# Optimization experiments

Hardware: AMD Instinct MI355X
Metric: run time of the kernel (lower is better)

The kernel has to match this reference:

```python
import jax, jax.numpy as jnp
import numpy as np

B, S, D_MODEL, D_FF, E, K = 4, 2048, 1024, 4096, 8, 2
CAP_FACTOR = 1.0


def setup_inputs() -> dict:
    key = jax.random.key(0)
    ks = jax.random.split(key, 6)
    std = 0.02
    return {
        "x": jax.random.normal(ks[0], (B, S, D_MODEL), jnp.float32),
        "router_w": jax.random.normal(ks[1], (E, D_MODEL), jnp.float32) * std,  # Linear(d_model,E,bias=False) weight
        "w1": jax.random.normal(ks[2], (E, D_MODEL, D_FF), jnp.float32) * std,
        "b1": jnp.zeros((E, D_FF), jnp.float32),
        "w2": jax.random.normal(ks[3], (E, D_FF, D_MODEL), jnp.float32) * std,
        "b2": jnp.zeros((E, D_MODEL), jnp.float32),
    }


def reference(x, router_w, w1, b1, w2, b2):
    b, s, d = x.shape
    T = b * s
    e = router_w.shape[0]
    capacity = int(CAP_FACTOR * T / e)  # static
    xf = x.reshape(T, d)

    # --- routing ---
    logits = xf @ router_w.T                       # [T,E]
    probs = jax.nn.softmax(logits, axis=-1)
    vals, idx = jax.lax.top_k(probs, K)            # [T,K] values / expert ids
    vals = vals / vals.sum(-1, keepdims=True)

    # dense gate matrix [T,E]; top_k experts are distinct so this is a scatter of K weights per token
    ar = jnp.arange(T)
    gates = jnp.zeros((T, e), x.dtype).at[ar[:, None], idx].add(vals)

    # --- load-balancing loss ---
    counts = jnp.zeros((e,), jnp.float32).at[idx.reshape(-1)].add(1.0)
    ideal = T * K / e
    lb_loss = jnp.sum((counts - ideal) ** 2) / (T ** 2)

    # --- capacity-limited dispatch (first `capacity` tokens in token order per expert) ---
    mask = gates > 0                                               # [T,E]
    order = jnp.argsort(jnp.logical_not(mask), axis=0)[:capacity]  # stable: assigned tokens first, ascending token id -> [cap,E]
    valid = jnp.take_along_axis(mask, order, axis=0)               # [cap,E] token actually assigned & within capacity
    idx_ec = order.T                                               # [E,cap]

    # --- grouped expert MLP ---
    xg = xf[idx_ec]                                                # [E,cap,D]
    h = jax.nn.gelu(jnp.einsum('ecd,edf->ecf', xg, w1) + b1[:, None, :], approximate=False)
    y = jnp.einsum('ecf,efd->ecd', h, w2) + b2[:, None, :]         # [E,cap,D]

    # --- combine (scatter-add with routing weights; dropped/invalid slots get weight 0) ---
    wt = gates[idx_ec, jnp.arange(e)[:, None]] * valid.T           # [E,cap]
    out = jnp.zeros((T, d), x.dtype).at[idx_ec.reshape(-1)].add((y * wt[..., None]).reshape(-1, d))
    return out.reshape(b, s, d), lb_loss
```

## Files before the change

kernel.cpp:

```cpp
#include <hip/hip_runtime.h>
#include <hip/hip_bf16.h>

#define T_TOK 8192
#define DMODEL 1024
#define DFF 4096
#define NEXP 8
#define CAP 1024

typedef __attribute__((ext_vector_type(8))) __bf16 bf16x8;
typedef __attribute__((ext_vector_type(4))) float f32x4;

__device__ __forceinline__ unsigned short f2bf(float f) {
  union { float f; unsigned int u; } v;
  v.f = f;
  return (unsigned short)((v.u + 0x7fffu + ((v.u >> 16) & 1u)) >> 16);
}

__device__ __forceinline__ float bfbits2f(unsigned int lo16) {
  union { unsigned int u; float f; } v; v.u = lo16 << 16; return v.f;
}

__device__ __forceinline__ float fast_gelu(float v) {
  float x = fabsf(v) * 0.70710678118654752440f;
  float t = __builtin_amdgcn_rcpf(1.0f + 0.3275911f * x);
  float poly = t * (0.254829592f + t * (-0.284496736f + t * (1.421413741f +
               t * (-1.453152027f + t * 1.061405429f))));
  float er = 1.0f - poly * __expf(-x * x);
  float s = (v >= 0.0f) ? er : -er;
  return 0.5f * v * (1.0f + s);
}

__device__ __forceinline__ void load_lds16(const unsigned short* g, unsigned short* l) {
  __builtin_amdgcn_global_load_lds((const __attribute__((address_space(1))) void*)g,
                                   (__attribute__((address_space(3))) void*)l,
                                   16, 0, 0);
}

__global__ void k_router(const float* __restrict__ x, const float* __restrict__ rw,
                         unsigned short* __restrict__ xb,
                         int* __restrict__ tk_idx, float* __restrict__ tk_w,
                         int* __restrict__ tinv) {
  if (threadIdx.x < 8) tinv[blockIdx.x * 8 + threadIdx.x] = -1;
  int wv = threadIdx.x >> 6, lane = threadIdx.x & 63;
  int t = blockIdx.x * 4 + wv;
  const float4* xr = (const float4*)(x + (size_t)t * DMODEL);
  uint2* xbw = (uint2*)(xb + (size_t)t * DMODEL);
  float acc[NEXP];
#pragma unroll
  for (int e = 0; e < NEXP; ++e) acc[e] = 0.f;
#pragma unroll
  for (int j = 0; j < DMODEL / 256; ++j) {
    float4 v = xr[j * 64 + lane];
#pragma unroll
    for (int e = 0; e < NEXP; ++e) {
      float4 w = ((const float4*)(rw + e * DMODEL))[j * 64 + lane];
      acc[e] += v.x * w.x + v.y * w.y + v.z * w.z + v.w * w.w;
    }
    uint2 p;
    p.x = (unsigned int)f2bf(v.x) | ((unsigned int)f2bf(v.y) << 16);
    p.y = (unsigned int)f2bf(v.z) | ((unsigned int)f2bf(v.w) << 16);
    xbw[j * 64 + lane] = p;
  }
#pragma unroll
  for (int e = 0; e < NEXP; ++e)
    for (int off = 32; off; off >>= 1) acc[e] += __shfl_xor(acc[e], off);
  if (lane == 0) {
    int i0 = 0;
    for (int e = 1; e < NEXP; ++e) if (acc[e] > acc[i0]) i0 = e;
    int i1 = (i0 == 0) ? 1 : 0;
    for (int e = 0; e < NEXP; ++e) if (e != i0 && acc[e] > acc[i1]) i1 = e;
    float ex = expf(acc[i1] - acc[i0]);
    float w0 = 1.f / (1.f + ex);
    float w1 = ex / (1.f + ex);
    tk_idx[2 * t] = i0; tk_idx[2 * t + 1] = i1;
    tk_w[2 * t] = w0;  tk_w[2 * t + 1] = w1;
  }
}

__global__ void k_transpose_cvt(const float* __restrict__ src, unsigned short* __restrict__ dst,
                                int Kd, int Nd) {
  __shared__ unsigned short tile[64][73];
  int e = blockIdx.z;
  size_t k0 = (size_t)blockIdx.y * 64, n0 = (size_t)blockIdx.x * 64;
  int tid = threadIdx.x;
  const float* sb = src + (size_t)e * Kd * Nd;
  int r = tid >> 4, cg = (tid & 15) * 4;
  for (int rr = 0; rr < 4; ++rr) {
    int row = r + rr * 16;
    float4 v = *(const float4*)(sb + (k0 + row) * Nd + n0 + cg);
    tile[row][cg + 0] = f2bf(v.x);
    tile[row][cg + 1] = f2bf(v.y);
    tile[row][cg + 2] = f2bf(v.z);
    tile[row][cg + 3] = f2bf(v.w);
  }
  __syncthreads();
  unsigned short* db = dst + (size_t)e * Nd * Kd;
  int rn = tid >> 3, kg = (tid & 7) * 8;
  for (int rr = 0; rr < 2; ++rr) {
    int nrow = rn + rr * 32;
    union { unsigned short h[8]; uint4 v; } o;
#pragma unroll
    for (int j = 0; j < 8; ++j) o.h[j] = tile[kg + j][nrow];
    *(uint4*)(db + (n0 + nrow) * Kd + k0 + kg) = o.v;
  }
}

__global__ void k_scan(const int* __restrict__ tk_idx, const float* __restrict__ tk_w,
                       int* __restrict__ etok, float* __restrict__ egate,
                       int* __restrict__ tinv, int* __restrict__ counts) {
  __shared__ int wavecnt[16], waveoff[16];
  __shared__ int soff;
  int e = blockIdx.x;
  int tid = threadIdx.x, lane = tid & 63, wv = tid >> 6;
  for (int i = tid; i < CAP; i += 1024) etok[e * CAP + i] = 0;
  if (tid == 0) soff = 0;
  __syncthreads();
  unsigned long long lt = (1ULL << lane) - 1ULL;
  for (int c = 0; c < T_TOK / 1024; ++c) {
    int t = c * 1024 + tid;
    int e0 = tk_idx[2 * t], e1 = tk_idx[2 * t + 1];
    bool is0 = (e0 == e), is1 = (e1 == e);
    bool mine = is0 || is1;
    unsigned long long bal = __ballot(mine);
    int pos = __popcll(bal & lt);
    if (lane == 0) wavecnt[wv] = __popcll(bal);
    __syncthreads();
    if (tid == 0) {
      int s = soff;
      for (int w = 0; w < 16; ++w) { waveoff[w] = s; s += wavecnt[w]; }
      soff = s;
    }
    __syncthreads();
    if (mine) {
      int r = waveoff[wv] + pos;
      if (r < CAP) {
        etok[e * CAP + r] = t;
        egate[e * CAP + r] = is0 ? tk_w[2 * t] : tk_w[2 * t + 1];
        tinv[2 * t + (is1 ? 1 : 0)] = e * CAP + r;
      }
    }
    __syncthreads();
  }
  if (tid == 0) counts[e] = soff;
}

__global__ __launch_bounds__(256) void k_gemm1(
    const unsigned short* __restrict__ xb, const unsigned short* __restrict__ w1t,
    const float* __restrict__ b1, const int* __restrict__ etok,
    unsigned short* __restrict__ H) {
  __shared__ __align__(16) unsigned short smem[8192];
  unsigned short* As = smem;
  unsigned short* Bs = smem + 4096;
  int tid = threadIdx.x;
  int lane = tid & 63, wv = tid >> 6;
  int bid = blockIdx.x;
  int e = bid >> 8;
  int b = bid & 255;
  int nl = b & 7, m = (b >> 3) & 7, nh = b >> 6;
  int m0 = m * 128, n0 = (nh * 8 + nl) * 128;

  const unsigned short* gA[2];
  const unsigned short* gB[2];
  unsigned short* lA[2];
  unsigned short* lB[2];
#pragma unroll
  for (int s = 0; s < 2; ++s) {
    int i = s * 256 + tid;
    int row = i >> 2, cb = (i & 3) * 8;
    int tok = etok[e * CAP + m0 + row];
    gA[s] = xb + (size_t)tok * DMODEL + cb;
    gB[s] = w1t + ((size_t)e * DFF + n0 + row) * DMODEL + cb;
    int wb = (s * 256 + wv * 64) * 8;
    lA[s] = As + wb;
    lB[s] = Bs + wb;
  }

  f32x4 zero = {0.f, 0.f, 0.f, 0.f};
  f32x4 acc[4][4];
#pragma unroll
  for (int mi = 0; mi < 4; ++mi)
#pragma unroll
    for (int ni = 0; ni < 4; ++ni) acc[mi][ni] = zero;

  int wm = (wv >> 1) * 64, wn = (wv & 1) * 64;
  int fr = lane & 15, quad = lane >> 4;
  const unsigned short* pa = As + (wm + fr) * 32 + quad * 8;
  const unsigned short* pb = Bs + (wn + fr) * 32 + quad * 8;

  for (int k0 = 0; k0 < DMODEL; k0 += 32) {
#pragma unroll
    for (int s = 0; s < 2; ++s) {
      load_lds16(gA[s] + k0, lA[s]);
      load_lds16(gB[s] + k0, lB[s]);
    }
    __syncthreads();
    bf16x8 av[4], bv[4];
#pragma unroll
    for (int mi = 0; mi < 4; ++mi) av[mi] = *(const bf16x8*)(pa + mi * 16 * 32);
#pragma unroll
    for (int ni = 0; ni < 4; ++ni) bv[ni] = *(const bf16x8*)(pb + ni * 16 * 32);
#pragma unroll
    for (int mi = 0; mi < 4; ++mi)
#pragma unroll
      for (int ni = 0; ni < 4; ++ni)
        acc[mi][ni] = __builtin_amdgcn_mfma_f32_16x16x32_bf16(bv[ni], av[mi], acc[mi][ni], 0, 0, 0);
    __syncthreads();
  }

  unsigned short* EP = smem + wv * 1536;
#pragma unroll
  for (int ni = 0; ni < 4; ++ni) {
    float4 b4 = *(const float4*)(b1 + e * DFF + n0 + wn + ni * 16 + quad * 4);
#pragma unroll
    for (int mi = 0; mi < 4; ++mi) {
      float v0 = fast_gelu(acc[mi][ni][0] + b4.x);
      float v1 = fast_gelu(acc[mi][ni][1] + b4.y);
      float v2 = fast_gelu(acc[mi][ni][2] + b4.z);
      float v3 = fast_gelu(acc[mi][ni][3] + b4.w);
      uint2 p;
      p.x = (unsigned int)f2bf(v0) | ((unsigned int)f2bf(v1) << 16);
      p.y = (unsigned int)f2bf(v2) | ((unsigned int)f2bf(v3) << 16);
      *(uint2*)(EP + (mi * 16 + fr) * 24 + quad * 4) = p;
    }
#pragma unroll
    for (int t = 0; t < 2; ++t) {
      int row = t * 32 + (lane >> 1), chunk = lane & 1;
      uint4 v = *(const uint4*)(EP + row * 24 + chunk * 8);
      *(uint4*)(H + ((size_t)e * CAP + m0 + wm + row) * DFF + n0 + wn + ni * 16 + chunk * 8) = v;
    }
  }
}

__global__ __launch_bounds__(256) void k_gemm2(
    const unsigned short* __restrict__ H, const unsigned short* __restrict__ w2t,
    const float* __restrict__ b2, unsigned short* __restrict__ Y) {
  __shared__ __align__(16) unsigned short smem[8192];
  unsigned short* As = smem;
  unsigned short* Bs = smem + 4096;
  int tid = threadIdx.x;
  int lane = tid & 63, wv = tid >> 6;
  int bid = blockIdx.x;
  int e = bid >> 6;
  int m0 = ((bid >> 3) & 7) * 128;
  int n0 = (bid & 7) * 128;

  const unsigned short* gA[2];
  const unsigned short* gB[2];
  unsigned short* lA[2];
  unsigned short* lB[2];
#pragma unroll
  for (int s = 0; s < 2; ++s) {
    int i = s * 256 + tid;
    int row = i >> 2, cb = (i & 3) * 8;
    gA[s] = H + ((size_t)e * CAP + m0 + row) * DFF + cb;
    gB[s] = w2t + ((size_t)e * DMODEL + n0 + row) * DFF + cb;
    int wb = (s * 256 + wv * 64) * 8;
    lA[s] = As + wb;
    lB[s] = Bs + wb;
  }

  f32x4 zero = {0.f, 0.f, 0.f, 0.f};
  f32x4 acc[4][4];
#pragma unroll
  for (int mi = 0; mi < 4; ++mi)
#pragma unroll
    for (int ni = 0; ni < 4; ++ni) acc[mi][ni] = zero;

  int wm = (wv >> 1) * 64, wn = (wv & 1) * 64;
  int fr = lane & 15, quad = lane >> 4;
  const unsigned short* pa = As + (wm + fr) * 32 + quad * 8;
  const unsigned short* pb = Bs + (wn + fr) * 32 + quad * 8;

  for (int k0 = 0; k0 < DFF; k0 += 32) {
#pragma unroll
    for (int s = 0; s < 2; ++s) {
      load_lds16(gA[s] + k0, lA[s]);
      load_lds16(gB[s] + k0, lB[s]);
    }
    __syncthreads();
    bf16x8 av[4], bv[4];
#pragma unroll
    for (int mi = 0; mi < 4; ++mi) av[mi] = *(const bf16x8*)(pa + mi * 16 * 32);
#pragma unroll
    for (int ni = 0; ni < 4; ++ni) bv[ni] = *(const bf16x8*)(pb + ni * 16 * 32);
#pragma unroll
    for (int mi = 0; mi < 4; ++mi)
#pragma unroll
      for (int ni = 0; ni < 4; ++ni)
        acc[mi][ni] = __builtin_amdgcn_mfma_f32_16x16x32_bf16(bv[ni], av[mi], acc[mi][ni], 0, 0, 0);
    __syncthreads();
  }

  unsigned short* EP = smem + wv * 1536;
#pragma unroll
  for (int ni = 0; ni < 4; ++ni) {
    float4 b4 = *(const float4*)(b2 + e * DMODEL + n0 + wn + ni * 16 + quad * 4);
#pragma unroll
    for (int mi = 0; mi < 4; ++mi) {
      uint2 p;
      p.x = (unsigned int)f2bf(acc[mi][ni][0] + b4.x) |
            ((unsigned int)f2bf(acc[mi][ni][1] + b4.y) << 16);
      p.y = (unsigned int)f2bf(acc[mi][ni][2] + b4.z) |
            ((unsigned int)f2bf(acc[mi][ni][3] + b4.w) << 16);
      *(uint2*)(EP + (mi * 16 + fr) * 24 + quad * 4) = p;
    }
#pragma unroll
    for (int t = 0; t < 2; ++t) {
      int row = t * 32 + (lane >> 1), chunk = lane & 1;
      uint4 v = *(const uint4*)(EP + row * 24 + chunk * 8);
      *(uint4*)(Y + ((size_t)e * CAP + m0 + wm + row) * DMODEL + n0 + wn + ni * 16 + chunk * 8) = v;
    }
  }
}

__global__ void k_combine(const unsigned short* __restrict__ Y,
                          const float* __restrict__ egate,
                          const int* __restrict__ tinv,
                          const int* __restrict__ counts,
                          float* __restrict__ out, float* __restrict__ loss_out) {
  int t = blockIdx.x, tid = threadIdx.x;
  int s0 = tinv[2 * t], s1 = tinv[2 * t + 1];
  int d0 = tid * 4;
  float a0 = 0.f, a1 = 0.f, a2 = 0.f, a3 = 0.f;
  if (s0 >= 0) {
    float g = egate[s0];
    uint2 v = *(const uint2*)(Y + (size_t)s0 * DMODEL + d0);
    a0 += g * bfbits2f(v.x & 0xffff); a1 += g * bfbits2f(v.x >> 16);
    a2 += g * bfbits2f(v.y & 0xffff); a3 += g * bfbits2f(v.y >> 16);
  }
  if (s1 >= 0) {
    float g = egate[s1];
    uint2 v = *(const uint2*)(Y + (size_t)s1 * DMODEL + d0);
    a0 += g * bfbits2f(v.x & 0xffff); a1 += g * bfbits2f(v.x >> 16);
    a2 += g * bfbits2f(v.y & 0xffff); a3 += g * bfbits2f(v.y >> 16);
  }
  float4 o = {a0, a1, a2, a3};
  *(float4*)(out + (size_t)t * DMODEL + d0) = o;
  if (t == 0 && tid == 0) {
    float loss = 0.f;
    for (int e = 0; e < NEXP; ++e) {
      float d = (float)counts[e] - 2048.0f;
      loss += d * d;
    }
    loss_out[0] = loss / (8192.0f * 8192.0f);
  }
}

extern "C" void kernel_launch(void* const* d_in, const int* in_sizes, int n_in,
                              void* d_out, int out_size, void* d_ws, size_t ws_size,
                              hipStream_t stream) {
  (void)in_sizes; (void)n_in; (void)ws_size; (void)out_size;
  const float* x  = (const float*)d_in[0];
  const float* rw = (const float*)d_in[1];
  const float* w1 = (const float*)d_in[2];
  const float* b1 = (const float*)d_in[3];
  const float* w2 = (const float*)d_in[4];
  const float* b2 = (const float*)d_in[5];
  float* out = (float*)d_out;

  char* ws = (char*)d_ws;
  const size_t XB_BYTES = (size_t)T_TOK * DMODEL * 2;
  const size_t WT_BYTES = (size_t)NEXP * DFF * DMODEL * 2;
  const size_t H_BYTES  = (size_t)NEXP * CAP * DFF * 2;
  unsigned short* xb = (unsigned short*)ws;
  unsigned short* Yb = xb;
  unsigned short* wT = (unsigned short*)(ws + XB_BYTES);
  unsigned short* Hb = (unsigned short*)(ws + XB_BYTES + WT_BYTES);
  char* small = ws + XB_BYTES + WT_BYTES + H_BYTES;
  int*   etok   = (int*)small;
  float* egate  = (float*)(small + NEXP * CAP * 4);
  int*   tkidx  = (int*)(small + 2 * NEXP * CAP * 4);
  float* tkw    = (float*)(small + 2 * NEXP * CAP * 4 + T_TOK * 2 * 4);
  int*   tinv   = (int*)(small + 2 * NEXP * CAP * 4 + 2 * T_TOK * 2 * 4);
  int*   counts = (int*)(small + 2 * NEXP * CAP * 4 + 3 * T_TOK * 2 * 4);

  k_router<<<T_TOK / 4, 256, 0, stream>>>(x, rw, xb, tkidx, tkw, tinv);
  k_scan<<<NEXP, 1024, 0, stream>>>(tkidx, tkw, etok, egate, tinv, counts);
  k_transpose_cvt<<<dim3(DFF / 64, DMODEL / 64, NEXP), 256, 0, stream>>>(w1, wT, DMODEL, DFF);
  k_gemm1<<<NEXP * 256, 256, 0, stream>>>(xb, wT, b1, etok, Hb);
  k_transpose_cvt<<<dim3(DMODEL / 64, DFF / 64, NEXP), 256, 0, stream>>>(w2, wT, DFF, DMODEL);
  k_gemm2<<<NEXP * 64, 256, 0, stream>>>(Hb, wT, b2, Yb);
  k_combine<<<T_TOK, 256, 0, stream>>>(Yb, egate, tinv, counts, out,
                                       out + (size_t)T_TOK * DMODEL);
}
```

Before: 558.4 us.

## Double-buffer LDS, swizzle tiles, reorder blocks by expert, and single-pass scan

```diff
diff --git a/kernel.cpp b/kernel.cpp
--- a/kernel.cpp
+++ b/kernel.cpp
@@ -108,71 +108,72 @@
 __global__ void k_scan(const int* __restrict__ tk_idx, const float* __restrict__ tk_w,
                        int* __restrict__ etok, float* __restrict__ egate,
                        int* __restrict__ tinv, int* __restrict__ counts) {
-  __shared__ int wavecnt[16], waveoff[16];
-  __shared__ int soff;
+  __shared__ int wavecnt[8][16];
+  __shared__ int waveoff[8][16];
   int e = blockIdx.x;
   int tid = threadIdx.x, lane = tid & 63, wv = tid >> 6;
   for (int i = tid; i < CAP; i += 1024) etok[e * CAP + i] = 0;
-  if (tid == 0) soff = 0;
-  __syncthreads();
   unsigned long long lt = (1ULL << lane) - 1ULL;
-  for (int c = 0; c < T_TOK / 1024; ++c) {
+  int pos[8], wh[8];
+  bool mine[8];
+#pragma unroll
+  for (int c = 0; c < 8; ++c) {
     int t = c * 1024 + tid;
     int e0 = tk_idx[2 * t], e1 = tk_idx[2 * t + 1];
     bool is0 = (e0 == e), is1 = (e1 == e);
-    bool mine = is0 || is1;
-    unsigned long long bal = __ballot(mine);
-    int pos = __popcll(bal & lt);
-    if (lane == 0) wavecnt[wv] = __popcll(bal);
-    __syncthreads();
-    if (tid == 0) {
-      int s = soff;
-      for (int w = 0; w < 16; ++w) { waveoff[w] = s; s += wavecnt[w]; }
-      soff = s;
-    }
-    __syncthreads();
-    if (mine) {
-      int r = waveoff[wv] + pos;
+    mine[c] = is0 || is1;
+    wh[c] = is1 ? 1 : 0;
+    unsigned long long bal = __ballot(mine[c]);
+    pos[c] = __popcll(bal & lt);
+    if (lane == 0) wavecnt[c][wv] = __popcll(bal);
+  }
+  __syncthreads();
+  if (tid == 0) {
+    int s = 0;
+    for (int c = 0; c < 8; ++c)
+      for (int w = 0; w < 16; ++w) { waveoff[c][w] = s; s += wavecnt[c][w]; }
+    counts[e] = s;
+  }
+  __syncthreads();
+#pragma unroll
+  for (int c = 0; c < 8; ++c) {
+    if (mine[c]) {
+      int t = c * 1024 + tid;
+      int r = waveoff[c][wv] + pos[c];
       if (r < CAP) {
         etok[e * CAP + r] = t;
-        egate[e * CAP + r] = is0 ? tk_w[2 * t] : tk_w[2 * t + 1];
-        tinv[2 * t + (is1 ? 1 : 0)] = e * CAP + r;
+        egate[e * CAP + r] = tk_w[2 * t + wh[c]];
+        tinv[2 * t + wh[c]] = e * CAP + r;
       }
     }
-    __syncthreads();
-  }
-  if (tid == 0) counts[e] = soff;
+  }
 }
 
 __global__ __launch_bounds__(256) void k_gemm1(
     const unsigned short* __restrict__ xb, const unsigned short* __restrict__ w1t,
     const float* __restrict__ b1, const int* __restrict__ etok,
     unsigned short* __restrict__ H) {
-  __shared__ __align__(16) unsigned short smem[8192];
-  unsigned short* As = smem;
-  unsigned short* Bs = smem + 4096;
+  __shared__ __align__(16) unsigned short smem[16384];
   int tid = threadIdx.x;
   int lane = tid & 63, wv = tid >> 6;
   int bid = blockIdx.x;
-  int e = bid >> 8;
-  int b = bid & 255;
-  int nl = b & 7, m = (b >> 3) & 7, nh = b >> 6;
-  int m0 = m * 128, n0 = (nh * 8 + nl) * 128;
+  int e = bid & 7;
+  int r = bid >> 3;
+  int n0 = (r & 31) * 128;
+  int m0 = (r >> 5) * 128;
 
   const unsigned short* gA[2];
   const unsigned short* gB[2];
-  unsigned short* lA[2];
-  unsigned short* lB[2];
+  int wb[2];
 #pragma unroll
   for (int s = 0; s < 2; ++s) {
     int i = s * 256 + tid;
-    int row = i >> 2, cb = (i & 3) * 8;
+    int row = i >> 2;
+    int q = (i & 3) ^ ((i >> 3) & 3);
     int tok = etok[e * CAP + m0 + row];
-    gA[s] = xb + (size_t)tok * DMODEL + cb;
-    gB[s] = w1t + ((size_t)e * DFF + n0 + row) * DMODEL + cb;
-    int wb = (s * 256 + wv * 64) * 8;
-    lA[s] = As + wb;
-    lB[s] = Bs + wb;
+    gA[s] = xb + (size_t)tok * DMODEL + q * 8;
+    gB[s] = w1t + ((size_t)e * DFF + n0 + row) * DMODEL + q * 8;
+    wb[s] = (s * 256 + wv * 64) * 8;
   }
 
   f32x4 zero = {0.f, 0.f, 0.f, 0.f};
@@ -184,28 +185,41 @@
 
   int wm = (wv >> 1) * 64, wn = (wv & 1) * 64;
   int fr = lane & 15, quad = lane >> 4;
-  const unsigned short* pa = As + (wm + fr) * 32 + quad * 8;
-  const unsigned short* pb = Bs + (wn + fr) * 32 + quad * 8;
-
-  for (int k0 = 0; k0 < DMODEL; k0 += 32) {
-#pragma unroll
-    for (int s = 0; s < 2; ++s) {
-      load_lds16(gA[s] + k0, lA[s]);
-      load_lds16(gB[s] + k0, lB[s]);
-    }
+  int cs = (quad ^ ((fr >> 1) & 3)) * 8;
+  int aoff = (wm + fr) * 32 + cs;
+  int boff = (wn + fr) * 32 + cs;
+
+#pragma unroll
+  for (int s = 0; s < 2; ++s) {
+    load_lds16(gA[s], smem + wb[s]);
+    load_lds16(gB[s], smem + 4096 + wb[s]);
+  }
+  int buf = 0;
+  for (int k0 = 32; k0 <= DMODEL; k0 += 32) {
     __syncthreads();
+    int nbuf = buf ^ 8192;
+    if (k0 < DMODEL) {
+#pragma unroll
+      for (int s = 0; s < 2; ++s) {
+        load_lds16(gA[s] + k0, smem + nbuf + wb[s]);
+        load_lds16(gB[s] + k0, smem + nbuf + 4096 + wb[s]);
+      }
+    }
+    const unsigned short* Ab = smem + buf;
+    const unsigned short* Bb = Ab + 4096;
     bf16x8 av[4], bv[4];
 #pragma unroll
-    for (int mi = 0; mi < 4; ++mi) av[mi] = *(const bf16x8*)(pa + mi * 16 * 32);
-#pragma unroll
-    for (int ni = 0; ni < 4; ++ni) bv[ni] = *(const bf16x8*)(pb + ni * 16 * 32);
+    for (int mi = 0; mi < 4; ++mi) av[mi] = *(const bf16x8*)(Ab + aoff + mi * 512);
+#pragma unroll
+    for (int ni = 0; ni < 4; ++ni) bv[ni] = *(const bf16x8*)(Bb + boff + ni * 512);
 #pragma unroll
     for (int mi = 0; mi < 4; ++mi)
 #pragma unroll
       for (int ni = 0; ni < 4; ++ni)
         acc[mi][ni] = __builtin_amdgcn_mfma_f32_16x16x32_bf16(bv[ni], av[mi], acc[mi][ni], 0, 0, 0);
-    __syncthreads();
-  }
+    buf = nbuf;
+  }
+  __syncthreads();
 
   unsigned short* EP = smem + wv * 1536;
 #pragma unroll
@@ -234,29 +248,26 @@
 __global__ __launch_bounds__(256) void k_gemm2(
     const unsigned short* __restrict__ H, const unsigned short* __restrict__ w2t,
     const float* __restrict__ b2, unsigned short* __restrict__ Y) {
-  __shared__ __align__(16) unsigned short smem[8192];
-  unsigned short* As = smem;
-  unsigned short* Bs = smem + 4096;
+  __shared__ __align__(16) unsigned short smem[16384];
   int tid = threadIdx.x;
   int lane = tid & 63, wv = tid >> 6;
   int bid = blockIdx.x;
-  int e = bid >> 6;
-  int m0 = ((bid >> 3) & 7) * 128;
-  int n0 = (bid & 7) * 128;
+  int e = bid & 7;
+  int r = bid >> 3;
+  int n0 = (r & 7) * 128;
+  int m0 = (r >> 3) * 128;
 
   const unsigned short* gA[2];
   const unsigned short* gB[2];
-  unsigned short* lA[2];
-  unsigned short* lB[2];
+  int wb[2];
 #pragma unroll
   for (int s = 0; s < 2; ++s) {
     int i = s * 256 + tid;
-    int row = i >> 2, cb = (i & 3) * 8;
-    gA[s] = H + ((size_t)e * CAP + m0 + row) * DFF + cb;
-    gB[s] = w2t + ((size_t)e * DMODEL + n0 + row) * DFF + cb;
-    int wb = (s * 256 + wv * 64) * 8;
-    lA[s] = As + wb;
-    lB[s] = Bs + wb;
+    int row = i >> 2;
+    int q = (i & 3) ^ ((i >> 3) & 3);
+    gA[s] = H + ((size_t)e * CAP + m0 + row) * DFF + q * 8;
+    gB[s] = w2t + ((size_t)e * DMODEL + n0 + row) * DFF + q * 8;
+    wb[s] = (s * 256 + wv * 64) * 8;
   }
 
   f32x4 zero = {0.f, 0.f, 0.f, 0.f};
@@ -268,28 +279,41 @@
 
   int wm = (wv >> 1) * 64, wn = (wv & 1) * 64;
   int fr = lane & 15, quad = lane >> 4;
-  const unsigned short* pa = As + (wm + fr) * 32 + quad * 8;
-  const unsigned short* pb = Bs + (wn + fr) * 32 + quad * 8;
-
-  for (int k0 = 0; k0 < DFF; k0 += 32) {
-#pragma unroll
-    for (int s = 0; s < 2; ++s) {
-      load_lds16(gA[s] + k0, lA[s]);
-      load_lds16(gB[s] + k0, lB[s]);
-    }
+  int cs = (quad ^ ((fr >> 1) & 3)) * 8;
+  int aoff = (wm + fr) * 32 + cs;
+  int boff = (wn + fr) * 32 + cs;
+
+#pragma unroll
+  for (int s = 0; s < 2; ++s) {
+    load_lds16(gA[s], smem + wb[s]);
+    load_lds16(gB[s], smem + 4096 + wb[s]);
+  }
+  int buf = 0;
+  for (int k0 = 32; k0 <= DFF; k0 += 32) {
     __syncthreads();
+    int nbuf = buf ^ 8192;
+    if (k0 < DFF) {
+#pragma unroll
+      for (int s = 0; s < 2; ++s) {
+        load_lds16(gA[s] + k0, smem + nbuf + wb[s]);
+        load_lds16(gB[s] + k0, smem + nbuf + 4096 + wb[s]);
+      }
+    }
+    const unsigned short* Ab = smem + buf;
+    const unsigned short* Bb = Ab + 4096;
     bf16x8 av[4], bv[4];
 #pragma unroll
-    for (int mi = 0; mi < 4; ++mi) av[mi] = *(const bf16x8*)(pa + mi * 16 * 32);
-#pragma unroll
-    for (int ni = 0; ni < 4; ++ni) bv[ni] = *(const bf16x8*)(pb + ni * 16 * 32);
+    for (int mi = 0; mi < 4; ++mi) av[mi] = *(const bf16x8*)(Ab + aoff + mi * 512);
+#pragma unroll
+    for (int ni = 0; ni < 4; ++ni) bv[ni] = *(const bf16x8*)(Bb + boff + ni * 512);
 #pragma unroll
     for (int mi = 0; mi < 4; ++mi)
 #pragma unroll
       for (int ni = 0; ni < 4; ++ni)
         acc[mi][ni] = __builtin_amdgcn_mfma_f32_16x16x32_bf16(bv[ni], av[mi], acc[mi][ni], 0, 0, 0);
-    __syncthreads();
-  }
+    buf = nbuf;
+  }
+  __syncthreads();
 
   unsigned short* EP = smem + wv * 1536;
 #pragma unroll
```

After: 541.9 us. 3.0% less time.
